# Performance work log

Measured on AMD Instinct MI355X. Metric: run time of the kernel, lower is better.

## Reference

```python
import jax, jax.numpy as jnp
import numpy as np

B, N, D_IN, D_OUT = 64, 512, 128, 128
LEAKY_SLOPE = 0.2  # DGL GATConv default negative_slope


def setup_inputs() -> dict:
    key = jax.random.key(0)
    k1, k2, k3, k4, k5 = jax.random.split(key, 5)
    embedding = jax.random.normal(k1, (B, N, D_IN), dtype=jnp.float32)
    W = jax.random.normal(k2, (D_IN, D_OUT), dtype=jnp.float32) / np.sqrt(D_IN)
    attn_l = jax.random.normal(k3, (D_OUT,), dtype=jnp.float32) * 0.1
    attn_r = jax.random.normal(k4, (D_OUT,), dtype=jnp.float32) * 0.1
    bias = jax.random.normal(k5, (D_OUT,), dtype=jnp.float32) * 0.01
    return {"embedding": embedding, "W": W, "attn_l": attn_l, "attn_r": attn_r, "bias": bias}


def reference(embedding, W, attn_l, attn_r, bias):
    # --- constructure_graph: per-sample adjacency E @ E^T thresholded at its
    # scalar mean, plus self-loops. edge (i, j): src=i (row), dst=j (col).
    scores = jnp.einsum('bnd,bmd->bnm', embedding, embedding)        # [B,N,N]
    thresh = jnp.mean(scores, axis=(1, 2), keepdims=True)            # scalar per sample
    self_loop = jnp.eye(scores.shape[1], dtype=bool)                  # [N,N]
    mask = (scores > thresh) | self_loop                              # [B,src,dst]

    # --- GATConv (1 head, eval mode: feat_drop/attn_drop are identity)
    z = jnp.einsum('bnd,de->bne', embedding, W)                       # [B,N,D_OUT]
    el = z @ attn_l                                                   # [B,N] source term
    er = z @ attn_r                                                   # [B,N] dest term
    e = jax.nn.leaky_relu(el[:, :, None] + er[:, None, :], LEAKY_SLOPE)  # [B,src,dst]
    e = jnp.where(mask, e, -jnp.inf)
    alpha = jax.nn.softmax(e, axis=1)                                 # softmax over incoming (src) edges per dst
    h = jnp.einsum('bij,bid->bjd', alpha, z)                          # aggregate src -> dst
    h = jax.nn.elu(h + bias)                                          # bias + activation=F.elu

    # --- mean pool over nodes
    return jnp.mean(h, axis=1)                                        # [B, D_OUT]
```

## Files before the change

kernel.cpp:

```cpp
#include <hip/hip_runtime.h>
#include <math.h>

#define BATCH 64
#define NN 512
#define DD 128
#define SLOPE 0.2f

typedef unsigned short u16;
typedef short bf16x8 __attribute__((ext_vector_type(8)));
typedef u16 u16x4 __attribute__((ext_vector_type(4)));
typedef u16 u16x8 __attribute__((ext_vector_type(8)));
typedef float f32x4 __attribute__((ext_vector_type(4)));

static __device__ __forceinline__ u16 f2bf(float x) {
    unsigned int u = __float_as_uint(x);
    return (u16)((u + 0x7fffu + ((u >> 16) & 1u)) >> 16);
}
static __device__ __forceinline__ float bf2f(u16 h) {
    return __uint_as_float(((unsigned int)h) << 16);
}
static __device__ __forceinline__ void gld16(const u16* g, u16* lds) {
    __builtin_amdgcn_global_load_lds(
        (const __attribute__((address_space(1))) unsigned int*)g,
        (__attribute__((address_space(3))) unsigned int*)lds, 16, 0, 0);
}

__global__ __launch_bounds__(256) void k_prep(const float* __restrict__ W,
                                              const float* __restrict__ E,
                                              u16* __restrict__ WtHi,
                                              u16* __restrict__ WtLo,
                                              float* __restrict__ cs2,
                                              float* __restrict__ out) {
    __shared__ float csr[8][128];
    int t = threadIdx.x;
    if (blockIdx.x == 0) {
        int n = t & 127, half = t >> 7;
        #pragma unroll
        for (int g = 0; g < 8; ++g) {
            u16x8 hv, lv;
            #pragma unroll
            for (int j = 0; j < 8; ++j) {
                float v = W[(size_t)(half * 64 + g * 8 + j) * DD + n];
                u16 h = f2bf(v);
                hv[j] = h;
                lv[j] = f2bf(v - bf2f(h));
            }
            *(u16x8*)&WtHi[(size_t)n * DD + half * 64 + g * 8] = hv;
            *(u16x8*)&WtLo[(size_t)n * DD + half * 64 + g * 8] = lv;
        }
    } else {
        int b = (blockIdx.x - 1) >> 1;
        int half = (blockIdx.x - 1) & 1;
        int c4 = t & 31, r0 = t >> 5;
        const float* Eb = E + ((size_t)b * NN + half * 256) * DD;
        float cp0 = 0.f, cp1 = 0.f, cp2 = 0.f, cp3 = 0.f;
        for (int k = 0; k < 32; ++k) {
            int row = r0 + k * 8;
            float4 v = *(const float4*)&Eb[(size_t)row * DD + c4 * 4];
            cp0 += v.x; cp1 += v.y; cp2 += v.z; cp3 += v.w;
        }
        csr[r0][c4 * 4 + 0] = cp0;
        csr[r0][c4 * 4 + 1] = cp1;
        csr[r0][c4 * 4 + 2] = cp2;
        csr[r0][c4 * 4 + 3] = cp3;
        if (t < 64) out[b * DD + half * 64 + t] = 0.f;
        __syncthreads();
        if (t < 128) {
            float s = 0.f;
            #pragma unroll
            for (int g = 0; g < 8; ++g) s += csr[g][t];
            cs2[(size_t)half * BATCH * DD + b * DD + t] = s;
        }
    }
}

__global__ __launch_bounds__(512) void k_z(const float* __restrict__ E,
                                           const u16* __restrict__ WtHi,
                                           const u16* __restrict__ WtLo,
                                           const float* __restrict__ al,
                                           const float* __restrict__ ar,
                                           u16* __restrict__ Ebf,
                                           u16* __restrict__ zT,
                                           float* __restrict__ el,
                                           float* __restrict__ er) {
    int bid = blockIdx.x;
    int b = (bid & 7) * 8 + (bid >> 5);
    int rg = (bid >> 3) & 3;
    int t = threadIdx.x;
    int w = t >> 6;
    int lane = t & 63;
    int l15 = lane & 15;
    int quad = lane >> 4;
    int sg = w >> 1;
    int ch = w & 1;

    __shared__ float elp_s[128], erp_s[128];
    for (int i = t; i < 128; i += 512) { elp_s[i] = 0.f; erp_s[i] = 0.f; }
    __syncthreads();

    bf16x8 bh[4][4], bl[4][4];
    float a_l[4], a_r[4];
    #pragma unroll
    for (int c = 0; c < 4; ++c) {
        int nt = ch * 4 + c;
        #pragma unroll
        for (int ks = 0; ks < 4; ++ks) {
            bh[c][ks] = *(const bf16x8*)(WtHi + (size_t)(nt * 16 + l15) * DD + ks * 32 + quad * 8);
            bl[c][ks] = *(const bf16x8*)(WtLo + (size_t)(nt * 16 + l15) * DD + ks * 32 + quad * 8);
        }
        a_l[c] = al[nt * 16 + l15];
        a_r[c] = ar[nt * 16 + l15];
    }

    #pragma unroll
    for (int si = 0; si < 2; ++si) {
        int s = sg * 2 + si;
        int row = rg * 128 + s * 16 + l15;
        const float* Er = E + ((size_t)b * NN + row) * DD;

        bf16x8 ah[4], alo[4];
        #pragma unroll
        for (int ks = 0; ks < 4; ++ks) {
            float4 v0 = *(const float4*)(Er + ks * 32 + quad * 8);
            float4 v1 = *(const float4*)(Er + ks * 32 + quad * 8 + 4);
            float vv[8] = {v0.x, v0.y, v0.z, v0.w, v1.x, v1.y, v1.z, v1.w};
            u16x8 hv, lv;
            #pragma unroll
            for (int j = 0; j < 8; ++j) {
                u16 h = f2bf(vv[j]);
                hv[j] = h;
                lv[j] = f2bf(vv[j] - bf2f(h));
            }
            ah[ks] = (bf16x8)hv;
            alo[ks] = (bf16x8)lv;
            if (ch == 0)
                *(u16x8*)&Ebf[((size_t)b * NN + row) * DD + ks * 32 + quad * 8] = hv;
        }

        f32x4 C[4];
        #pragma unroll
        for (int c = 0; c < 4; ++c) C[c] = (f32x4){0.f, 0.f, 0.f, 0.f};
        #pragma unroll
        for (int ks = 0; ks < 4; ++ks)
            #pragma unroll
            for (int c = 0; c < 4; ++c) {
                C[c] = __builtin_amdgcn_mfma_f32_16x16x32_bf16(ah[ks],  bh[c][ks], C[c], 0, 0, 0);
                C[c] = __builtin_amdgcn_mfma_f32_16x16x32_bf16(alo[ks], bh[c][ks], C[c], 0, 0, 0);
                C[c] = __builtin_amdgcn_mfma_f32_16x16x32_bf16(ah[ks],  bl[c][ks], C[c], 0, 0, 0);
            }

        float elp[4] = {0.f, 0.f, 0.f, 0.f};
        float erp[4] = {0.f, 0.f, 0.f, 0.f};
        #pragma unroll
        for (int c = 0; c < 4; ++c) {
            u16x4 zp;
            #pragma unroll
            for (int r = 0; r < 4; ++r) {
                zp[r] = f2bf(C[c][r]);
                elp[r] += C[c][r] * a_l[c];
                erp[r] += C[c][r] * a_r[c];
            }
            *(u16x4*)&zT[((size_t)b * DD + (ch * 4 + c) * 16 + l15) * NN
                         + rg * 128 + s * 16 + quad * 4] = zp;
        }
        #pragma unroll
        for (int r = 0; r < 4; ++r) {
            float vl = elp[r], vr = erp[r];
            #pragma unroll
            for (int off = 8; off > 0; off >>= 1) {
                vl += __shfl_down(vl, off);
                vr += __shfl_down(vr, off);
            }
            if (l15 == 0) {
                atomicAdd(&elp_s[s * 16 + quad * 4 + r], vl);
                atomicAdd(&erp_s[s * 16 + quad * 4 + r], vr);
            }
        }
    }
    __syncthreads();
    if (t < 128) {
        el[b * NN + rg * 128 + t] = elp_s[t];
        er[b * NN + rg * 128 + t] = erp_s[t];
    }
}

__global__ __launch_bounds__(256, 3) void k_main(const u16* __restrict__ Ebf,
                                                 const u16* __restrict__ zT,
                                                 const float* __restrict__ el,
                                                 const float* __restrict__ er,
                                                 const float* __restrict__ cs2,
                                                 const float* __restrict__ bias,
                                                 float* __restrict__ out) {
    int bid = blockIdx.x;
    int b = (bid & 7) * 8 + (bid >> 6);
    int j0 = ((bid >> 3) & 7) * 64;
    int t = threadIdx.x;
    int w = t >> 6;
    int lane = t & 63;
    int l15 = lane & 15;
    int quad = lane >> 4;
    int jb = j0 + w * 16;

    const u16* Eb = Ebf + (size_t)b * NN * DD;
    const u16* zTb = zT + (size_t)b * DD * NN;

    __shared__ u16 Ei[64 * DD];
    __shared__ u16 zTile[DD * 64];
    __shared__ u16 pT[4][16][72];
    __shared__ float tred[2];

    if (t < 128) {
        float c = cs2[b * DD + t] + cs2[BATCH * DD + b * DD + t];
        float v = c * c;
        #pragma unroll
        for (int off = 32; off > 0; off >>= 1) v += __shfl_down(v, off);
        if ((t & 63) == 0) tred[t >> 6] = v;
    }

    bf16x8 bEj[4];
    #pragma unroll
    for (int ks = 0; ks < 4; ++ks)
        bEj[ks] = *(const bf16x8*)(Eb + (size_t)(jb + l15) * DD + ks * 32 + quad * 8);
    float er_v = er[b * NN + jb + l15];

    f32x4 H[8];
    #pragma unroll
    for (int nt = 0; nt < 8; ++nt) H[nt] = (f32x4){0.f, 0.f, 0.f, 0.f};
    f32x4 CZ = (f32x4){0.f, 0.f, 0.f, 0.f};
    bf16x8 one8;
    #pragma unroll
    for (int j = 0; j < 8; ++j) one8[j] = (short)0x3F80;

    __syncthreads();
    float thr = (tred[0] + tred[1]) * (1.0f / ((float)NN * (float)NN));

    for (int c = 0; c < 8; ++c) {
        int i0 = c * 64;

        #pragma unroll
        for (int g = 0; g < 4; ++g) {
            const u16* gp = Eb + (size_t)(i0 + w * 16 + g * 4 + (lane >> 4)) * DD + (lane & 15) * 8;
            gld16(gp, &Ei[(w * 16 + g * 4) * DD]);
        }
        #pragma unroll
        for (int g = 0; g < 4; ++g) {
            const u16* gp = zTb + (size_t)(w * 32 + g * 8 + (lane >> 3)) * NN + i0 + (lane & 7) * 8;
            gld16(gp, &zTile[(w * 32 + g * 8) * 64]);
        }
        __syncthreads();

        #pragma unroll
        for (int it = 0; it < 4; ++it) {
            bf16x8 aE[4];
            #pragma unroll
            for (int ks = 0; ks < 4; ++ks)
                aE[ks] = *(const bf16x8*)&Ei[(it * 16 + l15) * DD + ks * 32 + quad * 8];
            f32x4 S = (f32x4){0.f, 0.f, 0.f, 0.f};
            #pragma unroll
            for (int ks = 0; ks < 4; ++ks)
                S = __builtin_amdgcn_mfma_f32_16x16x32_bf16(aE[ks], bEj[ks], S, 0, 0, 0);

            float4 el4 = *(const float4*)(el + b * NN + i0 + it * 16 + quad * 4);
            float elv[4] = {el4.x, el4.y, el4.z, el4.w};
            u16x4 pk;
            if (i0 + it * 16 == jb) {
                #pragma unroll
                for (int r = 0; r < 4; ++r) {
                    float x = elv[r] + er_v;
                    float lg = x > 0.f ? x : SLOPE * x;
                    bool keep = (S[r] > thr) || ((quad * 4 + r) == l15);
                    pk[r] = f2bf(keep ? __expf(lg) : 0.f);
                }
            } else {
                #pragma unroll
                for (int r = 0; r < 4; ++r) {
                    float x = elv[r] + er_v;
                    float lg = x > 0.f ? x : SLOPE * x;
                    pk[r] = f2bf((S[r] > thr) ? __expf(lg) : 0.f);
                }
            }
            *(u16x4*)&pT[w][l15][it * 16 + quad * 4] = pk;
        }

        bf16x8 ap[2];
        #pragma unroll
        for (int ks = 0; ks < 2; ++ks)
            ap[ks] = *(const bf16x8*)&pT[w][l15][ks * 32 + quad * 8];

        #pragma unroll
        for (int ks = 0; ks < 2; ++ks) {
            CZ = __builtin_amdgcn_mfma_f32_16x16x32_bf16(ap[ks], one8, CZ, 0, 0, 0);
            #pragma unroll
            for (int nt = 0; nt < 8; ++nt) {
                bf16x8 bz = *(const bf16x8*)&zTile[(nt * 16 + l15) * 64 + ks * 32 + quad * 8];
                H[nt] = __builtin_amdgcn_mfma_f32_16x16x32_bf16(ap[ks], bz, H[nt], 0, 0, 0);
            }
        }
        __syncthreads();
    }

    float zinv[4];
    #pragma unroll
    for (int r = 0; r < 4; ++r) zinv[r] = 1.0f / CZ[r];

    #pragma unroll
    for (int nt = 0; nt < 8; ++nt) {
        float bsv = bias[nt * 16 + l15];
        float acc = 0.f;
        #pragma unroll
        for (int r = 0; r < 4; ++r) {
            float v = H[nt][r] * zinv[r] + bsv;
            v = v > 0.f ? v : (__expf(v) - 1.f);
            acc += v;
        }
        acc += __shfl_down(acc, 32);
        acc += __shfl_down(acc, 16);
        if (lane < 16) atomicAdd(&out[b * DD + nt * 16 + lane], acc * (1.0f / NN));
    }
}

extern "C" void kernel_launch(void* const* d_in, const int* in_sizes, int n_in,
                              void* d_out, int out_size, void* d_ws, size_t ws_size,
                              hipStream_t stream) {
    const float* E    = (const float*)d_in[0];
    const float* W    = (const float*)d_in[1];
    const float* al   = (const float*)d_in[2];
    const float* ar   = (const float*)d_in[3];
    const float* bias = (const float*)d_in[4];
    float* out = (float*)d_out;

    u16* Ebf = (u16*)d_ws;
    u16* zTb = Ebf + (size_t)BATCH * NN * DD;
    u16* WtHi = zTb + (size_t)BATCH * NN * DD;
    u16* WtLo = WtHi + (size_t)DD * DD;
    float* el  = (float*)(WtLo + (size_t)DD * DD);
    float* er  = el + (size_t)BATCH * NN;
    float* cs2 = er + (size_t)BATCH * NN;

    k_prep<<<dim3(129), dim3(256), 0, stream>>>(W, E, WtHi, WtLo, cs2, out);
    k_z<<<dim3(256), dim3(512), 0, stream>>>(E, WtHi, WtLo, al, ar, Ebf, zTb, el, er);
    k_main<<<dim3(512), dim3(256), 0, stream>>>(Ebf, zTb, el, er, cs2, bias, out);
}
```

Before: 125.5 us.

## Fuse prep, projection and attention kernels into one cooperative kernel with grid sync

Merges the three launches into a single cooperative kernel of 256 blocks × 512 threads. Phase one computes per-block column sums, splits W into bf16 hi/lo parts inside each block, and produces z, el and er. A grid-wide sync then leads into the attention/aggregation phase. The attention phase now uses 8 waves per block over 128 destination columns, instead of 512 blocks of 4 waves. This removes two launch gaps and the separate W-transpose pass, at the cost of redundant W conversion in every block, grid-sync overhead, and fewer, larger blocks in the main phase (256 instead of 512).

Measured after the change: 231.0 us. 84.1% more time.

```diff
diff --git a/kernel.cpp b/kernel.cpp
--- a/kernel.cpp
+++ b/kernel.cpp
@@ -1,5 +1,8 @@
 #include <hip/hip_runtime.h>
+#include <hip/hip_cooperative_groups.h>
 #include <math.h>
+
+namespace cg = cooperative_groups;
 
 #define BATCH 64
 #define NN 512
@@ -25,297 +28,271 @@
         (__attribute__((address_space(3))) unsigned int*)lds, 16, 0, 0);
 }
 
-__global__ __launch_bounds__(256) void k_prep(const float* __restrict__ W,
-                                              const float* __restrict__ E,
-                                              u16* __restrict__ WtHi,
-                                              u16* __restrict__ WtLo,
-                                              float* __restrict__ cs2,
-                                              float* __restrict__ out) {
-    __shared__ float csr[8][128];
-    int t = threadIdx.x;
-    if (blockIdx.x == 0) {
-        int n = t & 127, half = t >> 7;
-        #pragma unroll
-        for (int g = 0; g < 8; ++g) {
-            u16x8 hv, lv;
-            #pragma unroll
-            for (int j = 0; j < 8; ++j) {
-                float v = W[(size_t)(half * 64 + g * 8 + j) * DD + n];
-                u16 h = f2bf(v);
-                hv[j] = h;
-                lv[j] = f2bf(v - bf2f(h));
-            }
-            *(u16x8*)&WtHi[(size_t)n * DD + half * 64 + g * 8] = hv;
-            *(u16x8*)&WtLo[(size_t)n * DD + half * 64 + g * 8] = lv;
-        }
-    } else {
-        int b = (blockIdx.x - 1) >> 1;
-        int half = (blockIdx.x - 1) & 1;
-        int c4 = t & 31, r0 = t >> 5;
-        const float* Eb = E + ((size_t)b * NN + half * 256) * DD;
-        float cp0 = 0.f, cp1 = 0.f, cp2 = 0.f, cp3 = 0.f;
-        for (int k = 0; k < 32; ++k) {
-            int row = r0 + k * 8;
-            float4 v = *(const float4*)&Eb[(size_t)row * DD + c4 * 4];
-            cp0 += v.x; cp1 += v.y; cp2 += v.z; cp3 += v.w;
-        }
-        csr[r0][c4 * 4 + 0] = cp0;
-        csr[r0][c4 * 4 + 1] = cp1;
-        csr[r0][c4 * 4 + 2] = cp2;
-        csr[r0][c4 * 4 + 3] = cp3;
-        if (t < 64) out[b * DD + half * 64 + t] = 0.f;
-        __syncthreads();
-        if (t < 128) {
-            float s = 0.f;
-            #pragma unroll
-            for (int g = 0; g < 8; ++g) s += csr[g][t];
-            cs2[(size_t)half * BATCH * DD + b * DD + t] = s;
-        }
-    }
-}
-
-__global__ __launch_bounds__(512) void k_z(const float* __restrict__ E,
-                                           const u16* __restrict__ WtHi,
-                                           const u16* __restrict__ WtLo,
-                                           const float* __restrict__ al,
-                                           const float* __restrict__ ar,
-                                           u16* __restrict__ Ebf,
-                                           u16* __restrict__ zT,
-                                           float* __restrict__ el,
-                                           float* __restrict__ er) {
+__global__ __launch_bounds__(512, 2) void k_all(
+    const float* __restrict__ E, const float* __restrict__ W,
+    const float* __restrict__ al, const float* __restrict__ ar,
+    const float* __restrict__ bias,
+    u16* __restrict__ Ebf, u16* __restrict__ zT,
+    float* __restrict__ el, float* __restrict__ er,
+    float* __restrict__ cs4, float* __restrict__ out)
+{
     int bid = blockIdx.x;
     int b = (bid & 7) * 8 + (bid >> 5);
-    int rg = (bid >> 3) & 3;
+    int sub = (bid >> 3) & 3;
     int t = threadIdx.x;
     int w = t >> 6;
     int lane = t & 63;
     int l15 = lane & 15;
     int quad = lane >> 4;
-    int sg = w >> 1;
-    int ch = w & 1;
-
+
+    __shared__ float csr[16][128];
     __shared__ float elp_s[128], erp_s[128];
-    for (int i = t; i < 128; i += 512) { elp_s[i] = 0.f; erp_s[i] = 0.f; }
-    __syncthreads();
-
-    bf16x8 bh[4][4], bl[4][4];
-    float a_l[4], a_r[4];
-    #pragma unroll
-    for (int c = 0; c < 4; ++c) {
-        int nt = ch * 4 + c;
-        #pragma unroll
-        for (int ks = 0; ks < 4; ++ks) {
-            bh[c][ks] = *(const bf16x8*)(WtHi + (size_t)(nt * 16 + l15) * DD + ks * 32 + quad * 8);
-            bl[c][ks] = *(const bf16x8*)(WtLo + (size_t)(nt * 16 + l15) * DD + ks * 32 + quad * 8);
-        }
-        a_l[c] = al[nt * 16 + l15];
-        a_r[c] = ar[nt * 16 + l15];
-    }
-
-    #pragma unroll
-    for (int si = 0; si < 2; ++si) {
-        int s = sg * 2 + si;
-        int row = rg * 128 + s * 16 + l15;
-        const float* Er = E + ((size_t)b * NN + row) * DD;
-
-        bf16x8 ah[4], alo[4];
-        #pragma unroll
-        for (int ks = 0; ks < 4; ++ks) {
-            float4 v0 = *(const float4*)(Er + ks * 32 + quad * 8);
-            float4 v1 = *(const float4*)(Er + ks * 32 + quad * 8 + 4);
-            float vv[8] = {v0.x, v0.y, v0.z, v0.w, v1.x, v1.y, v1.z, v1.w};
-            u16x8 hv, lv;
-            #pragma unroll
-            for (int j = 0; j < 8; ++j) {
-                u16 h = f2bf(vv[j]);
-                hv[j] = h;
-                lv[j] = f2bf(vv[j] - bf2f(h));
-            }
-            ah[ks] = (bf16x8)hv;
-            alo[ks] = (bf16x8)lv;
-            if (ch == 0)
-                *(u16x8*)&Ebf[((size_t)b * NN + row) * DD + ks * 32 + quad * 8] = hv;
-        }
-
-        f32x4 C[4];
-        #pragma unroll
-        for (int c = 0; c < 4; ++c) C[c] = (f32x4){0.f, 0.f, 0.f, 0.f};
-        #pragma unroll
-        for (int ks = 0; ks < 4; ++ks)
-            #pragma unroll
-            for (int c = 0; c < 4; ++c) {
-                C[c] = __builtin_amdgcn_mfma_f32_16x16x32_bf16(ah[ks],  bh[c][ks], C[c], 0, 0, 0);
-                C[c] = __builtin_amdgcn_mfma_f32_16x16x32_bf16(alo[ks], bh[c][ks], C[c], 0, 0, 0);
-                C[c] = __builtin_amdgcn_mfma_f32_16x16x32_bf16(ah[ks],  bl[c][ks], C[c], 0, 0, 0);
-            }
-
-        float elp[4] = {0.f, 0.f, 0.f, 0.f};
-        float erp[4] = {0.f, 0.f, 0.f, 0.f};
-        #pragma unroll
-        for (int c = 0; c < 4; ++c) {
-            u16x4 zp;
-            #pragma unroll
-            for (int r = 0; r < 4; ++r) {
-                zp[r] = f2bf(C[c][r]);
-                elp[r] += C[c][r] * a_l[c];
-                erp[r] += C[c][r] * a_r[c];
-            }
-            *(u16x4*)&zT[((size_t)b * DD + (ch * 4 + c) * 16 + l15) * NN
-                         + rg * 128 + s * 16 + quad * 4] = zp;
-        }
-        #pragma unroll
-        for (int r = 0; r < 4; ++r) {
-            float vl = elp[r], vr = erp[r];
-            #pragma unroll
-            for (int off = 8; off > 0; off >>= 1) {
-                vl += __shfl_down(vl, off);
-                vr += __shfl_down(vr, off);
-            }
-            if (l15 == 0) {
-                atomicAdd(&elp_s[s * 16 + quad * 4 + r], vl);
-                atomicAdd(&erp_s[s * 16 + quad * 4 + r], vr);
-            }
-        }
-    }
-    __syncthreads();
-    if (t < 128) {
-        el[b * NN + rg * 128 + t] = elp_s[t];
-        er[b * NN + rg * 128 + t] = erp_s[t];
-    }
-}
-
-__global__ __launch_bounds__(256, 3) void k_main(const u16* __restrict__ Ebf,
-                                                 const u16* __restrict__ zT,
-                                                 const float* __restrict__ el,
-                                                 const float* __restrict__ er,
-                                                 const float* __restrict__ cs2,
-                                                 const float* __restrict__ bias,
-                                                 float* __restrict__ out) {
-    int bid = blockIdx.x;
-    int b = (bid & 7) * 8 + (bid >> 6);
-    int j0 = ((bid >> 3) & 7) * 64;
-    int t = threadIdx.x;
-    int w = t >> 6;
-    int lane = t & 63;
-    int l15 = lane & 15;
-    int quad = lane >> 4;
-    int jb = j0 + w * 16;
-
-    const u16* Eb = Ebf + (size_t)b * NN * DD;
-    const u16* zTb = zT + (size_t)b * DD * NN;
-
     __shared__ u16 Ei[64 * DD];
     __shared__ u16 zTile[DD * 64];
-    __shared__ u16 pT[4][16][72];
+    __shared__ u16 pT[8][16][72];
     __shared__ float tred[2];
 
-    if (t < 128) {
-        float c = cs2[b * DD + t] + cs2[BATCH * DD + b * DD + t];
-        float v = c * c;
-        #pragma unroll
-        for (int off = 32; off > 0; off >>= 1) v += __shfl_down(v, off);
-        if ((t & 63) == 0) tred[t >> 6] = v;
+    {
+        int rg = sub;
+        for (int i = t; i < 128; i += 512) { elp_s[i] = 0.f; erp_s[i] = 0.f; }
+
+        int c4 = t & 31, r0 = t >> 5;
+        const float* Eb1 = E + ((size_t)b * NN + rg * 128) * DD;
+        float cp0 = 0.f, cp1 = 0.f, cp2 = 0.f, cp3 = 0.f;
+        #pragma unroll
+        for (int k = 0; k < 8; ++k) {
+            int row = r0 + k * 16;
+            float4 v = *(const float4*)&Eb1[(size_t)row * DD + c4 * 4];
+            cp0 += v.x; cp1 += v.y; cp2 += v.z; cp3 += v.w;
+        }
+        csr[r0][c4 * 4 + 0] = cp0;
+        csr[r0][c4 * 4 + 1] = cp1;
+        csr[r0][c4 * 4 + 2] = cp2;
+        csr[r0][c4 * 4 + 3] = cp3;
+        __syncthreads();
+        if (t < 128) {
+            float s = 0.f;
+            #pragma unroll
+            for (int g = 0; g < 16; ++g) s += csr[g][t];
+            cs4[((size_t)rg * BATCH + b) * DD + t] = s;
+            if (rg == 0) out[b * DD + t] = 0.f;
+        }
+
+        int ch = w & 1, sg = w >> 1;
+        bf16x8 bh[4][4], bl[4][4];
+        float a_l[4], a_r[4];
+        #pragma unroll
+        for (int c = 0; c < 4; ++c) {
+            int n = (ch * 4 + c) * 16 + l15;
+            #pragma unroll
+            for (int ks = 0; ks < 4; ++ks) {
+                u16x8 hv, lv;
+                #pragma unroll
+                for (int j = 0; j < 8; ++j) {
+                    float v = W[(size_t)(ks * 32 + quad * 8 + j) * DD + n];
+                    u16 h = f2bf(v);
+                    hv[j] = h;
+                    lv[j] = f2bf(v - bf2f(h));
+                }
+                bh[c][ks] = (bf16x8)hv;
+                bl[c][ks] = (bf16x8)lv;
+            }
+            a_l[c] = al[n];
+            a_r[c] = ar[n];
+        }
+
+        #pragma unroll
+        for (int si = 0; si < 2; ++si) {
+            int s = sg * 2 + si;
+            int row = rg * 128 + s * 16 + l15;
+            const float* Er = E + ((size_t)b * NN + row) * DD;
+
+            bf16x8 ah[4], alo[4];
+            #pragma unroll
+            for (int ks = 0; ks < 4; ++ks) {
+                float4 v0 = *(const float4*)(Er + ks * 32 + quad * 8);
+                float4 v1 = *(const float4*)(Er + ks * 32 + quad * 8 + 4);
+                float vv[8] = {v0.x, v0.y, v0.z, v0.w, v1.x, v1.y, v1.z, v1.w};
+                u16x8 hv, lv;
+                #pragma unroll
+                for (int j = 0; j < 8; ++j) {
+                    u16 h = f2bf(vv[j]);
+                    hv[j] = h;
+                    lv[j] = f2bf(vv[j] - bf2f(h));
+                }
+                ah[ks] = (bf16x8)hv;
+                alo[ks] = (bf16x8)lv;
+                if (ch == 0)
+                    *(u16x8*)&Ebf[((size_t)b * NN + row) * DD + ks * 32 + quad * 8] = hv;
+            }
+
+            f32x4 C[4];
+            #pragma unroll
+            for (int c = 0; c < 4; ++c) C[c] = (f32x4){0.f, 0.f, 0.f, 0.f};
+            #pragma unroll
+            for (int ks = 0; ks < 4; ++ks)
+                #pragma unroll
+                for (int c = 0; c < 4; ++c) {
+                    C[c] = __builtin_amdgcn_mfma_f32_16x16x32_bf16(ah[ks],  bh[c][ks], C[c], 0, 0, 0);
+                    C[c] = __builtin_amdgcn_mfma_f32_16x16x32_bf16(alo[ks], bh[c][ks], C[c], 0, 0, 0);
+                    C[c] = __builtin_amdgcn_mfma_f32_16x16x32_bf16(ah[ks],  bl[c][ks], C[c], 0, 0, 0);
+                }
+
+            float elp[4] = {0.f, 0.f, 0.f, 0.f};
+            float erp[4] = {0.f, 0.f, 0.f, 0.f};
+            #pragma unroll
+            for (int c = 0; c < 4; ++c) {
+                u16x4 zp;
+                #pragma unroll
+                for (int r = 0; r < 4; ++r) {
+                    zp[r] = f2bf(C[c][r]);
+                    elp[r] += C[c][r] * a_l[c];
+                    erp[r] += C[c][r] * a_r[c];
+                }
+                *(u16x4*)&zT[((size_t)b * DD + (ch * 4 + c) * 16 + l15) * NN
+                             + rg * 128 + s * 16 + quad * 4] = zp;
+            }
+            #pragma unroll
+            for (int r = 0; r < 4; ++r) {
+                float vl = elp[r], vr = erp[r];
+                #pragma unroll
+                for (int off = 8; off > 0; off >>= 1) {
+                    vl += __shfl_down(vl, off);
+                    vr += __shfl_down(vr, off);
+                }
+                if (l15 == 0) {
+                    atomicAdd(&elp_s[s * 16 + quad * 4 + r], vl);
+                    atomicAdd(&erp_s[s * 16 + quad * 4 + r], vr);
+                }
+            }
+        }
+        __syncthreads();
+        if (t < 128) {
+            el[b * NN + rg * 128 + t] = elp_s[t];
+            er[b * NN + rg * 128 + t] = erp_s[t];
+        }
     }
 
-    bf16x8 bEj[4];
-    #pragma unroll
-    for (int ks = 0; ks < 4; ++ks)
-        bEj[ks] = *(const bf16x8*)(Eb + (size_t)(jb + l15) * DD + ks * 32 + quad * 8);
-    float er_v = er[b * NN + jb + l15];
-
-    f32x4 H[8];
-    #pragma unroll
-    for (int nt = 0; nt < 8; ++nt) H[nt] = (f32x4){0.f, 0.f, 0.f, 0.f};
-    f32x4 CZ = (f32x4){0.f, 0.f, 0.f, 0.f};
-    bf16x8 one8;
-    #pragma unroll
-    for (int j = 0; j < 8; ++j) one8[j] = (short)0x3F80;
-
-    __syncthreads();
-    float thr = (tred[0] + tred[1]) * (1.0f / ((float)NN * (float)NN));
-
-    for (int c = 0; c < 8; ++c) {
-        int i0 = c * 64;
-
-        #pragma unroll
-        for (int g = 0; g < 4; ++g) {
-            const u16* gp = Eb + (size_t)(i0 + w * 16 + g * 4 + (lane >> 4)) * DD + (lane & 15) * 8;
-            gld16(gp, &Ei[(w * 16 + g * 4) * DD]);
-        }
-        #pragma unroll
-        for (int g = 0; g < 4; ++g) {
-            const u16* gp = zTb + (size_t)(w * 32 + g * 8 + (lane >> 3)) * NN + i0 + (lane & 7) * 8;
-            gld16(gp, &zTile[(w * 32 + g * 8) * 64]);
-        }
+    __threadfence();
+    cg::this_grid().sync();
+
+    {
+        int j0 = sub * 128;
+        int jb = j0 + w * 16;
+        const u16* Eb = Ebf + (size_t)b * NN * DD;
+        const u16* zTb = zT + (size_t)b * DD * NN;
+
+        if (t < 128) {
+            float cc = 0.f;
+            #pragma unroll
+            for (int rg = 0; rg < 4; ++rg)
+                cc += cs4[((size_t)rg * BATCH + b) * DD + t];
+            float v = cc * cc;
+            #pragma unroll
+            for (int off = 32; off > 0; off >>= 1) v += __shfl_down(v, off);
+            if ((t & 63) == 0) tred[t >> 6] = v;
+        }
+
+        bf16x8 bEj[4];
+        #pragma unroll
+        for (int ks = 0; ks < 4; ++ks)
+            bEj[ks] = *(const bf16x8*)(Eb + (size_t)(jb + l15) * DD + ks * 32 + quad * 8);
+        float er_v = er[b * NN + jb + l15];
+
+        f32x4 H[8];
+        #pragma unroll
+        for (int nt = 0; nt < 8; ++nt) H[nt] = (f32x4){0.f, 0.f, 0.f, 0.f};
+        f32x4 CZ = (f32x4){0.f, 0.f, 0.f, 0.f};
+        bf16x8 one8;
+        #pragma unroll
+        for (int j = 0; j < 8; ++j) one8[j] = (short)0x3F80;
+
         __syncthreads();
-
-        #pragma unroll
-        for (int it = 0; it < 4; ++it) {
-            bf16x8 aE[4];
-            #pragma unroll
-            for (int ks = 0; ks < 4; ++ks)
-                aE[ks] = *(const bf16x8*)&Ei[(it * 16 + l15) * DD + ks * 32 + quad * 8];
-            f32x4 S = (f32x4){0.f, 0.f, 0.f, 0.f};
-            #pragma unroll
-            for (int ks = 0; ks < 4; ++ks)
-                S = __builtin_amdgcn_mfma_f32_16x16x32_bf16(aE[ks], bEj[ks], S, 0, 0, 0);
-
-            float4 el4 = *(const float4*)(el + b * NN + i0 + it * 16 + quad * 4);
-            float elv[4] = {el4.x, el4.y, el4.z, el4.w};
-            u16x4 pk;
-            if (i0 + it * 16 == jb) {
-                #pragma unroll
-                for (int r = 0; r < 4; ++r) {
-                    float x = elv[r] + er_v;
-                    float lg = x > 0.f ? x : SLOPE * x;
-                    bool keep = (S[r] > thr) || ((quad * 4 + r) == l15);
-                    pk[r] = f2bf(keep ? __expf(lg) : 0.f);
-                }
-            } else {
-                #pragma unroll
-                for (int r = 0; r < 4; ++r) {
-                    float x = elv[r] + er_v;
-                    float lg = x > 0.f ? x : SLOPE * x;
-                    pk[r] = f2bf((S[r] > thr) ? __expf(lg) : 0.f);
-                }
-            }
-            *(u16x4*)&pT[w][l15][it * 16 + quad * 4] = pk;
-        }
-
-        bf16x8 ap[2];
-        #pragma unroll
-        for (int ks = 0; ks < 2; ++ks)
-            ap[ks] = *(const bf16x8*)&pT[w][l15][ks * 32 + quad * 8];
-
-        #pragma unroll
-        for (int ks = 0; ks < 2; ++ks) {
-            CZ = __builtin_amdgcn_mfma_f32_16x16x32_bf16(ap[ks], one8, CZ, 0, 0, 0);
-            #pragma unroll
-            for (int nt = 0; nt < 8; ++nt) {
-                bf16x8 bz = *(const bf16x8*)&zTile[(nt * 16 + l15) * 64 + ks * 32 + quad * 8];
-                H[nt] = __builtin_amdgcn_mfma_f32_16x16x32_bf16(ap[ks], bz, H[nt], 0, 0, 0);
-            }
-        }
-        __syncthreads();
-    }
-
-    float zinv[4];
-    #pragma unroll
-    for (int r = 0; r < 4; ++r) zinv[r] = 1.0f / CZ[r];
-
-    #pragma unroll
-    for (int nt = 0; nt < 8; ++nt) {
-        float bsv = bias[nt * 16 + l15];
-        float acc = 0.f;
-        #pragma unroll
-        for (int r = 0; r < 4; ++r) {
-            float v = H[nt][r] * zinv[r] + bsv;
-            v = v > 0.f ? v : (__expf(v) - 1.f);
-            acc += v;
-        }
-        acc += __shfl_down(acc, 32);
-        acc += __shfl_down(acc, 16);
-        if (lane < 16) atomicAdd(&out[b * DD + nt * 16 + lane], acc * (1.0f / NN));
+        float thr = (tred[0] + tred[1]) * (1.0f / ((float)NN * (float)NN));
+
+        for (int c = 0; c < 8; ++c) {
+            int i0 = c * 64;
+
+            #pragma unroll
+            for (int g = 0; g < 2; ++g) {
+                const u16* gp = Eb + (size_t)(i0 + w * 8 + g * 4 + (lane >> 4)) * DD + (lane & 15) * 8;
+                gld16(gp, &Ei[(w * 8 + g * 4) * DD]);
+            }
+            #pragma unroll
+            for (int g = 0; g < 2; ++g) {
+                const u16* gp = zTb + (size_t)(w * 16 + g * 8 + (lane >> 3)) * NN + i0 + (lane & 7) * 8;
+                gld16(gp, &zTile[(w * 16 + g * 8) * 64]);
+            }
+            __syncthreads();
+
+            #pragma unroll
+            for (int it = 0; it < 4; ++it) {
+                bf16x8 aE[4];
+                #pragma unroll
+                for (int ks = 0; ks < 4; ++ks)
+                    aE[ks] = *(const bf16x8*)&Ei[(it * 16 + l15) * DD + ks * 32 + quad * 8];
+                f32x4 S = (f32x4){0.f, 0.f, 0.f, 0.f};
+                #pragma unroll
+                for (int ks = 0; ks < 4; ++ks)
+                    S = __builtin_amdgcn_mfma_f32_16x16x32_bf16(aE[ks], bEj[ks], S, 0, 0, 0);
+
+                float4 el4 = *(const float4*)(el + b * NN + i0 + it * 16 + quad * 4);
+                float elv[4] = {el4.x, el4.y, el4.z, el4.w};
+                u16x4 pk;
+                if (i0 + it * 16 == jb) {
+                    #pragma unroll
+                    for (int r = 0; r < 4; ++r) {
+                        float x = elv[r] + er_v;
+                        float lg = x > 0.f ? x : SLOPE * x;
+                        bool keep = (S[r] > thr) || ((quad * 4 + r) == l15);
+                        pk[r] = f2bf(keep ? __expf(lg) : 0.f);
+                    }
+                } else {
+                    #pragma unroll
+                    for (int r = 0; r < 4; ++r) {
+                        float x = elv[r] + er_v;
+                        float lg = x > 0.f ? x : SLOPE * x;
+                        pk[r] = f2bf((S[r] > thr) ? __expf(lg) : 0.f);
+                    }
+                }
+                *(u16x4*)&pT[w][l15][it * 16 + quad * 4] = pk;
+            }
+
+            bf16x8 ap[2];
+            #pragma unroll
+            for (int ks = 0; ks < 2; ++ks)
+                ap[ks] = *(const bf16x8*)&pT[w][l15][ks * 32 + quad * 8];
+
+            #pragma unroll
+            for (int ks = 0; ks < 2; ++ks) {
+                CZ = __builtin_amdgcn_mfma_f32_16x16x32_bf16(ap[ks], one8, CZ, 0, 0, 0);
+                #pragma unroll
+                for (int nt = 0; nt < 8; ++nt) {
+                    bf16x8 bz = *(const bf16x8*)&zTile[(nt * 16 + l15) * 64 + ks * 32 + quad * 8];
+                    H[nt] = __builtin_amdgcn_mfma_f32_16x16x32_bf16(ap[ks], bz, H[nt], 0, 0, 0);
+                }
+            }
+            __syncthreads();
+        }
+
+        float zinv[4];
+        #pragma unroll
+        for (int r = 0; r < 4; ++r) zinv[r] = 1.0f / CZ[r];
+
+        #pragma unroll
+        for (int nt = 0; nt < 8; ++nt) {
+            float bsv = bias[nt * 16 + l15];
+            float acc = 0.f;
+            #pragma unroll
+            for (int r = 0; r < 4; ++r) {
+                float v = H[nt][r] * zinv[r] + bsv;
+                v = v > 0.f ? v : (__expf(v) - 1.f);
+                acc += v;
+            }
+            acc += __shfl_down(acc, 32);
+            acc += __shfl_down(acc, 16);
+            if (lane < 16) atomicAdd(&out[b * DD + nt * 16 + lane], acc * (1.0f / NN));
+        }
     }
 }
 
@@ -331,13 +308,13 @@
 
     u16* Ebf = (u16*)d_ws;
     u16* zTb = Ebf + (size_t)BATCH * NN * DD;
-    u16* WtHi = zTb + (size_t)BATCH * NN * DD;
-    u16* WtLo = WtHi + (size_t)DD * DD;
-    float* el  = (float*)(WtLo + (size_t)DD * DD);
+    float* el  = (float*)(zTb + (size_t)BATCH * NN * DD);
     float* er  = el + (size_t)BATCH * NN;
-    float* cs2 = er + (size_t)BATCH * NN;
-
-    k_prep<<<dim3(129), dim3(256), 0, stream>>>(W, E, WtHi, WtLo, cs2, out);
-    k_z<<<dim3(256), dim3(512), 0, stream>>>(E, WtHi, WtLo, al, ar, Ebf, zTb, el, er);
-    k_main<<<dim3(512), dim3(256), 0, stream>>>(Ebf, zTb, el, er, cs2, bias, out);
-}
+    float* cs4 = er + (size_t)BATCH * NN;
+
+    void* args[] = {(void*)&E, (void*)&W, (void*)&al, (void*)&ar, (void*)&bias,
+                    (void*)&Ebf, (void*)&zTb, (void*)&el, (void*)&er,
+                    (void*)&cs4, (void*)&out};
+    hipLaunchCooperativeKernel((const void*)k_all, dim3(256), dim3(512),
+                               args, 0, stream);
+}
```
